# Optimization experiments

Measured on AMD Instinct MI355X. Metric: run time of the kernel, lower is better.

Reference implementation:

```python
import jax, jax.numpy as jnp
import numpy as np

N_SRC = 50000
N_DST = 50000
E = 640000
D_IN = 128
D_OUT = 128
H = 4
D_HEAD = D_OUT // H


def setup_inputs() -> dict:
    key = jax.random.key(0)
    k1, k2, k3, k4, k5, k6 = jax.random.split(key, 6)
    src_feat = jax.random.normal(k1, (N_SRC, D_IN), dtype=jnp.float32)
    dst_feat = jax.random.normal(k2, (N_DST, D_IN), dtype=jnp.float32)
    src_idx = jax.random.randint(k3, (E,), 0, N_SRC)
    dst_idx = jax.random.randint(k4, (E,), 0, N_DST)
    edge_index = jnp.stack([src_idx, dst_idx], axis=0)  # [2, E]
    # nn.Linear(d_in, d_out, bias=False): store as [d_in, d_out] so h = x @ W
    W = jax.random.normal(k5, (D_IN, D_OUT), dtype=jnp.float32) * (1.0 / np.sqrt(D_IN))
    # nn.Linear(2*d_head, 1, bias=False): attention vector of length 2*d_head
    a = jax.random.normal(k6, (2 * D_HEAD,), dtype=jnp.float32) * (1.0 / np.sqrt(2 * D_HEAD))
    return {"src_feat": src_feat, "dst_feat": dst_feat, "edge_index": edge_index,
            "W": W, "a": a, "num_dst": N_DST}


def reference(src_feat, dst_feat, edge_index, W, a, num_dst):
    # Dropout in eval mode (identity).
    d_out = W.shape[1]
    d_head = d_out // H
    src_idx = edge_index[0]
    dst_idx = edge_index[1]

    h_src = (src_feat @ W).reshape(-1, H, d_head)  # [N_src, H, d_head]
    h_dst = (dst_feat @ W).reshape(-1, H, d_head)  # [N_dst, H, d_head]
    h_src_e = h_src[src_idx]                        # [E, H, d_head]
    h_dst_e = h_dst[dst_idx]                        # [E, H, d_head]

    # a^T [h_src || h_dst] == h_src . a_src + h_dst . a_dst (shared across heads)
    a_src, a_dst = a[:d_head], a[d_head:]
    e = jax.nn.elu(jnp.einsum('ehd,d->eh', h_src_e, a_src)
                   + jnp.einsum('ehd,d->eh', h_dst_e, a_dst))  # [E, H]

    # Segment softmax over edges grouped by destination node.
    e_max = jax.ops.segment_max(e, dst_idx, num_segments=num_dst)      # [N_dst, H]
    exp_e = jnp.exp(e - e_max[dst_idx])
    denom = jax.ops.segment_sum(exp_e, dst_idx, num_segments=num_dst)  # [N_dst, H]
    alpha = exp_e / (denom[dst_idx] + 1e-12)                           # [E, H]

    # Scatter-add of weighted messages.
    out = jax.ops.segment_sum(alpha[..., None] * h_src_e, dst_idx,
                              num_segments=num_dst)                    # [N_dst, H, d_head]
    return out.reshape(num_dst, d_out)
```

## Files before the change

kernel.cpp:

```cpp
#include <hip/hip_runtime.h>
#include <math.h>

constexpr int N_SRC_ = 50000;
constexpr int N_DST_ = 50000;
constexpr int N_TOT_ = 100000;
constexpr int E_     = 640000;
constexpr int D_     = 128;
constexpr int CAP_   = 64;
constexpr int NTILE  = (N_SRC_ + 31) / 32;
constexpr int MMB    = (NTILE + 3) / 4;
constexpr int NCHUNK = (E_ + 2047) / 2048;
constexpr int SCB    = NCHUNK * 8;
constexpr int DPR    = N_DST_ / 8;

typedef float f32x4  __attribute__((ext_vector_type(4)));
typedef short bf16x8 __attribute__((ext_vector_type(8)));

union U4 { unsigned int u[4]; bf16x8 v; };

static __device__ __forceinline__ unsigned short f2bf_rne(float f) {
    unsigned int x = __float_as_uint(f);
    return (unsigned short)((x + 0x7FFFu + ((x >> 16) & 1u)) >> 16);
}

__global__ __launch_bounds__(256) void k_prep(
    const float* __restrict__ W, const float* __restrict__ a,
    unsigned short* __restrict__ wt, float* __restrict__ va)
{
    int tid = blockIdx.x * 256 + threadIdx.x;
    if (tid >= 136 * 16) return;
    int n = tid >> 4, c = tid & 15;
    if (n < 128) {
        int slot = c ^ (n & 15);
        size_t base = (size_t)n * 128 + slot * 8;
#pragma unroll
        for (int j = 0; j < 8; ++j) {
            int k = c * 8 + j;
            wt[base + j] = f2bf_rne(W[(size_t)k * 128 + n]);
        }
    } else {
        int col = n - 128, half = col >> 2, hd = col & 3;
#pragma unroll
        for (int j = 0; j < 8; ++j) {
            int k = c * 8 + j;
            float acc = 0.f;
            for (int c2 = 0; c2 < 32; ++c2)
                acc += W[(size_t)k * 128 + hd * 32 + c2] * a[half * 32 + c2];
            va[(size_t)k * 8 + col] = acc;
        }
    }
}

__global__ __launch_bounds__(256) void k_s2(
    const float* __restrict__ src, const float* __restrict__ dst,
    const float* __restrict__ va, float* __restrict__ s)
{
    const int gw = (blockIdx.x * 256 + threadIdx.x) >> 6;
    const int lane = threadIdx.x & 63;
    const int l32 = lane & 31, hf = lane >> 5;

    float4 vs[4], vd[4];
#pragma unroll
    for (int j = 0; j < 4; ++j) {
        const float* vp = va + (size_t)(4 * l32 + j) * 8;
        vs[j] = *(const float4*)vp;
        vd[j] = *(const float4*)(vp + 4);
    }

    for (int p = gw; p < N_TOT_ / 2; p += 2048) {
        int node = p * 2 + hf;
        bool is_src = node < N_SRC_;
        const float* f = is_src ? src + (size_t)node * D_
                                : dst + (size_t)(node - N_SRC_) * D_;
        float4 x = *(const float4*)(f + l32 * 4);
        float4 v0 = is_src ? vs[0] : vd[0];
        float4 v1 = is_src ? vs[1] : vd[1];
        float4 v2 = is_src ? vs[2] : vd[2];
        float4 v3 = is_src ? vs[3] : vd[3];
        float a0 = x.x * v0.x + x.y * v1.x + x.z * v2.x + x.w * v3.x;
        float a1 = x.x * v0.y + x.y * v1.y + x.z * v2.y + x.w * v3.y;
        float a2 = x.x * v0.z + x.y * v1.z + x.z * v2.z + x.w * v3.z;
        float a3 = x.x * v0.w + x.y * v1.w + x.z * v2.w + x.w * v3.w;
#pragma unroll
        for (int m = 1; m < 32; m <<= 1) {
            a0 += __shfl_xor(a0, m, 64);
            a1 += __shfl_xor(a1, m, 64);
            a2 += __shfl_xor(a2, m, 64);
            a3 += __shfl_xor(a3, m, 64);
        }
        if (l32 == 0)
            *(float4*)&s[(size_t)node * 4] = make_float4(a0, a1, a2, a3);
    }
}

__global__ __launch_bounds__(256) void k_mms(
    const float* __restrict__ src, const unsigned short* __restrict__ wt,
    const int* __restrict__ src_idx, const int* __restrict__ dst_idx,
    const float* __restrict__ s,
    int* __restrict__ cursor, uint4* __restrict__ bucket,
    unsigned int* __restrict__ h)
{
    if (blockIdx.x >= MMB) {
        int bid = (int)blockIdx.x - MMB;
        int r = bid & 7;
        int ebase = (bid >> 3) * 2048 + threadIdx.x;
#pragma unroll
        for (int ii = 0; ii < 8; ++ii) {
            int e = ebase + ii * 256;
            if (e >= E_) break;
            int dn = dst_idx[e];
            if (dn / DPR != r) continue;
            int sn = src_idx[e];
            float4 vsv = *(const float4*)&s[(size_t)sn * 4];
            float4 vdv = *(const float4*)&s[(size_t)(N_SRC_ + dn) * 4];
            float x0 = vsv.x + vdv.x, x1 = vsv.y + vdv.y;
            float x2 = vsv.z + vdv.z, x3 = vsv.w + vdv.w;
            float w0 = __expf(x0 > 0.f ? x0 : (__expf(x0) - 1.f));
            float w1 = __expf(x1 > 0.f ? x1 : (__expf(x1) - 1.f));
            float w2 = __expf(x2 > 0.f ? x2 : (__expf(x2) - 1.f));
            float w3 = __expf(x3 > 0.f ? x3 : (__expf(x3) - 1.f));
            uint4 ent;
            ent.x = (unsigned int)sn;
            ent.y = (unsigned int)f2bf_rne(w0) | ((unsigned int)f2bf_rne(w1) << 16);
            ent.z = (unsigned int)f2bf_rne(w2) | ((unsigned int)f2bf_rne(w3) << 16);
            ent.w = 0u;
            int pos = atomicAdd(&cursor[dn], 1);
            if (pos < CAP_) bucket[(size_t)dn * CAP_ + pos] = ent;
        }
        return;
    }

    __shared__ unsigned short wl[128 * 128];
    const int t = threadIdx.x;
    {
        const float4* gw = (const float4*)wt;
        float4* sw = (float4*)wl;
#pragma unroll
        for (int i = 0; i < 8; ++i) sw[t + 256 * i] = gw[t + 256 * i];
    }
    __syncthreads();

    const int wid = t >> 6, lane = t & 63;
    const int g = lane >> 4, sidx = lane & 15;
    const int wtile = blockIdx.x * 4 + wid;
    if (wtile >= NTILE) return;
    const int base = wtile * 32;
    const int r0 = base + sidx;
    const int r1g = base + 16 + sidx;
    const int r1 = (r1g < N_SRC_) ? r1g : 0;
    const float* p0 = src + (size_t)r0 * D_;
    const float* p1 = src + (size_t)r1 * D_;

    f32x4 acc[2][8];
#pragma unroll
    for (int m = 0; m < 2; ++m)
#pragma unroll
        for (int nf = 0; nf < 8; ++nf) acc[m][nf] = (f32x4)0.f;

#pragma unroll
    for (int ks = 0; ks < 4; ++ks) {
        const int k0 = ks * 32 + g * 8;
        bf16x8 af[2];
#pragma unroll
        for (int m = 0; m < 2; ++m) {
            const float* p = m ? p1 : p0;
            float4 v0 = *(const float4*)(p + k0);
            float4 v1 = *(const float4*)(p + k0 + 4);
            float f[8] = {v0.x, v0.y, v0.z, v0.w, v1.x, v1.y, v1.z, v1.w};
            U4 P;
#pragma unroll
            for (int q = 0; q < 4; ++q)
                P.u[q] = (unsigned int)f2bf_rne(f[2 * q])
                       | ((unsigned int)f2bf_rne(f[2 * q + 1]) << 16);
            af[m] = P.v;
        }
#pragma unroll
        for (int nf = 0; nf < 8; ++nf) {
            const int n = nf * 16 + sidx;
            const int off = n * 128 + ((ks * 4 + g) ^ sidx) * 8;
            bf16x8 b = *(const bf16x8*)&wl[off];
            acc[0][nf] = __builtin_amdgcn_mfma_f32_16x16x32_bf16(af[0], b, acc[0][nf], 0, 0, 0);
            acc[1][nf] = __builtin_amdgcn_mfma_f32_16x16x32_bf16(af[1], b, acc[1][nf], 0, 0, 0);
        }
    }

#pragma unroll
    for (int m = 0; m < 2; ++m) {
        const int rowb = base + m * 16 + g * 4;
#pragma unroll
        for (int r = 0; r < 4; ++r) {
            const int row = rowb + r;
            if (row < N_SRC_) {
#pragma unroll
                for (int q = 0; q < 4; ++q) {
                    unsigned int val = (unsigned int)f2bf_rne(acc[m][2 * q][r])
                                     | ((unsigned int)f2bf_rne(acc[m][2 * q + 1][r]) << 16);
                    h[(size_t)row * 64 + q * 16 + sidx] = val;
                }
            }
        }
    }
}

__global__ __launch_bounds__(256) void k_gather(
    const unsigned int* __restrict__ h2, const int* __restrict__ cursor,
    const uint4* __restrict__ bucket, float* __restrict__ out)
{
    int wid = (blockIdx.x * 256 + threadIdx.x) >> 6;
    int lane = threadIdx.x & 63;
    if (wid >= N_DST_) return;
    int cnt = min(cursor[wid], CAP_);
    const int hd = lane >> 4;
    const int sub = lane & 15;
    const uint4* B = bucket + (size_t)wid * CAP_;

    auto wext = [&](const uint4& e) {
        unsigned int u = (hd & 2) ? e.z : e.y;
        return __uint_as_float((hd & 1) ? (u & 0xFFFF0000u) : (u << 16));
    };

    float2 A0 = make_float2(0.f, 0.f), A1 = A0, A2 = A0, A3 = A0;
    float d0 = 0.f, d1 = 0.f, d2 = 0.f, d3 = 0.f;
    int i = 0;
    for (; i + 4 <= cnt; i += 4) {
        uint4 e0 = B[i], e1 = B[i + 1], e2 = B[i + 2], e3 = B[i + 3];
        unsigned int v0 = h2[(size_t)e0.x * 64 + lane];
        unsigned int v1 = h2[(size_t)e1.x * 64 + lane];
        unsigned int v2 = h2[(size_t)e2.x * 64 + lane];
        unsigned int v3 = h2[(size_t)e3.x * 64 + lane];
        float w0 = wext(e0), w1 = wext(e1), w2 = wext(e2), w3 = wext(e3);
        d0 += w0; d1 += w1; d2 += w2; d3 += w3;
        A0.x = fmaf(w0, __uint_as_float(v0 << 16), A0.x);
        A0.y = fmaf(w0, __uint_as_float(v0 & 0xFFFF0000u), A0.y);
        A1.x = fmaf(w1, __uint_as_float(v1 << 16), A1.x);
        A1.y = fmaf(w1, __uint_as_float(v1 & 0xFFFF0000u), A1.y);
        A2.x = fmaf(w2, __uint_as_float(v2 << 16), A2.x);
        A2.y = fmaf(w2, __uint_as_float(v2 & 0xFFFF0000u), A2.y);
        A3.x = fmaf(w3, __uint_as_float(v3 << 16), A3.x);
        A3.y = fmaf(w3, __uint_as_float(v3 & 0xFFFF0000u), A3.y);
    }
    for (; i < cnt; ++i) {
        uint4 e = B[i];
        unsigned int v = h2[(size_t)e.x * 64 + lane];
        float w = wext(e);
        d0 += w;
        A0.x = fmaf(w, __uint_as_float(v << 16), A0.x);
        A0.y = fmaf(w, __uint_as_float(v & 0xFFFF0000u), A0.y);
    }

    float den = (d0 + d1) + (d2 + d3);
    float2 acc = make_float2((A0.x + A1.x) + (A2.x + A3.x),
                             (A0.y + A1.y) + (A2.y + A3.y));
    float inv = 1.f / (den + 1e-12f);
    out[(size_t)wid * D_ + 32 * hd + sub]      = acc.x * inv;
    out[(size_t)wid * D_ + 32 * hd + sub + 16] = acc.y * inv;
}

extern "C" void kernel_launch(void* const* d_in, const int* in_sizes, int n_in,
                              void* d_out, int out_size, void* d_ws, size_t ws_size,
                              hipStream_t stream)
{
    const float* src_feat = (const float*)d_in[0];
    const float* dst_feat = (const float*)d_in[1];
    const int*   edge     = (const int*)d_in[2];
    const int*   src_idx  = edge;
    const int*   dst_idx  = edge + E_;
    const float* W        = (const float*)d_in[3];
    const float* a        = (const float*)d_in[4];
    float*       out      = (float*)d_out;

    char* p = (char*)d_ws;
    auto alloc = [&](size_t bytes) {
        char* r = p;
        p += (bytes + 255) & ~(size_t)255;
        return r;
    };
    unsigned int* h    = (unsigned int*)alloc((size_t)N_SRC_ * 64 * 4);
    float*  s          = (float*)alloc((size_t)N_TOT_ * 4 * sizeof(float));
    int*    cursor     = (int*)alloc((size_t)N_DST_ * sizeof(int));
    uint4*  bucket     = (uint4*)alloc((size_t)N_DST_ * CAP_ * sizeof(uint4));
    unsigned short* wt = (unsigned short*)alloc((size_t)128 * 128 * 2);
    float*  va         = (float*)alloc((size_t)128 * 8 * sizeof(float));

    hipMemsetAsync(cursor, 0, (size_t)N_DST_ * sizeof(int), stream);

    k_prep<<<(136 * 16 + 255) / 256, 256, 0, stream>>>(W, a, wt, va);
    k_s2<<<512, 256, 0, stream>>>(src_feat, dst_feat, va, s);
    k_mms<<<MMB + SCB, 256, 0, stream>>>(src_feat, wt, src_idx, dst_idx, s,
                                         cursor, bucket, h);
    k_gather<<<(N_DST_ * 64 + 255) / 256, 256, 0, stream>>>(
        h, cursor, bucket, out);
}
```

Measured before the change: 216.7 us.

## Fold prep into projection kernels, split scatter out, deepen gather unroll

Removes the separate weight-prep kernel and the cursor memset. Each s2v block now recomputes W·a in shared memory and zeroes the cursors, and each matmul block converts W to swizzled bf16 in LDS directly. The edge scatter moves from a co-scheduled part of the matmul launch, which filtered edges by destination range over 8 passes, to its own one-edge-per-thread kernel, which cuts the redundant index reads. The gather loop is unrolled to 8 outstanding row loads. The cost is redundant per-block W·a and W-transpose work with strided global reads, and the scatter no longer overlaps the matmul.

```diff
diff --git a/kernel.cpp b/kernel.cpp
--- a/kernel.cpp
+++ b/kernel.cpp
@@ -9,9 +9,6 @@
 constexpr int CAP_   = 64;
 constexpr int NTILE  = (N_SRC_ + 31) / 32;
 constexpr int MMB    = (NTILE + 3) / 4;
-constexpr int NCHUNK = (E_ + 2047) / 2048;
-constexpr int SCB    = NCHUNK * 8;
-constexpr int DPR    = N_DST_ / 8;
 
 typedef float f32x4  __attribute__((ext_vector_type(4)));
 typedef short bf16x8 __attribute__((ext_vector_type(8)));
@@ -23,48 +20,38 @@
     return (unsigned short)((x + 0x7FFFu + ((x >> 16) & 1u)) >> 16);
 }
 
-__global__ __launch_bounds__(256) void k_prep(
+__global__ __launch_bounds__(256) void k_s2v(
+    const float* __restrict__ src, const float* __restrict__ dst,
     const float* __restrict__ W, const float* __restrict__ a,
-    unsigned short* __restrict__ wt, float* __restrict__ va)
-{
-    int tid = blockIdx.x * 256 + threadIdx.x;
-    if (tid >= 136 * 16) return;
-    int n = tid >> 4, c = tid & 15;
-    if (n < 128) {
-        int slot = c ^ (n & 15);
-        size_t base = (size_t)n * 128 + slot * 8;
-#pragma unroll
-        for (int j = 0; j < 8; ++j) {
-            int k = c * 8 + j;
-            wt[base + j] = f2bf_rne(W[(size_t)k * 128 + n]);
-        }
-    } else {
-        int col = n - 128, half = col >> 2, hd = col & 3;
-#pragma unroll
-        for (int j = 0; j < 8; ++j) {
-            int k = c * 8 + j;
-            float acc = 0.f;
-            for (int c2 = 0; c2 < 32; ++c2)
-                acc += W[(size_t)k * 128 + hd * 32 + c2] * a[half * 32 + c2];
-            va[(size_t)k * 8 + col] = acc;
-        }
-    }
-}
-
-__global__ __launch_bounds__(256) void k_s2(
-    const float* __restrict__ src, const float* __restrict__ dst,
-    const float* __restrict__ va, float* __restrict__ s)
-{
-    const int gw = (blockIdx.x * 256 + threadIdx.x) >> 6;
-    const int lane = threadIdx.x & 63;
+    float* __restrict__ s, int* __restrict__ cursor)
+{
+    __shared__ float val[128 * 8];
+    const int t = threadIdx.x;
+
+    int cid = blockIdx.x * 256 + t;
+    if (cid < N_DST_) cursor[cid] = 0;
+
+#pragma unroll
+    for (int j = 0; j < 4; ++j) {
+        int pair = t * 4 + j;
+        int k = pair >> 3, col = pair & 7;
+        int half = col >> 2, hd = col & 3;
+        float acc = 0.f;
+        for (int c2 = 0; c2 < 32; ++c2)
+            acc += W[(size_t)k * 128 + hd * 32 + c2] * a[half * 32 + c2];
+        val[k * 8 + col] = acc;
+    }
+    __syncthreads();
+
+    const int gw = (blockIdx.x * 256 + t) >> 6;
+    const int lane = t & 63;
     const int l32 = lane & 31, hf = lane >> 5;
 
     float4 vs[4], vd[4];
 #pragma unroll
     for (int j = 0; j < 4; ++j) {
-        const float* vp = va + (size_t)(4 * l32 + j) * 8;
-        vs[j] = *(const float4*)vp;
-        vd[j] = *(const float4*)(vp + 4);
+        vs[j] = *(const float4*)&val[(4 * l32 + j) * 8];
+        vd[j] = *(const float4*)&val[(4 * l32 + j) * 8 + 4];
     }
 
     for (int p = gw; p < N_TOT_ / 2; p += 2048) {
@@ -93,50 +80,28 @@
     }
 }
 
-__global__ __launch_bounds__(256) void k_mms(
-    const float* __restrict__ src, const unsigned short* __restrict__ wt,
-    const int* __restrict__ src_idx, const int* __restrict__ dst_idx,
-    const float* __restrict__ s,
-    int* __restrict__ cursor, uint4* __restrict__ bucket,
+__global__ __launch_bounds__(256) void k_mm(
+    const float* __restrict__ src, const float* __restrict__ W,
     unsigned int* __restrict__ h)
 {
-    if (blockIdx.x >= MMB) {
-        int bid = (int)blockIdx.x - MMB;
-        int r = bid & 7;
-        int ebase = (bid >> 3) * 2048 + threadIdx.x;
-#pragma unroll
-        for (int ii = 0; ii < 8; ++ii) {
-            int e = ebase + ii * 256;
-            if (e >= E_) break;
-            int dn = dst_idx[e];
-            if (dn / DPR != r) continue;
-            int sn = src_idx[e];
-            float4 vsv = *(const float4*)&s[(size_t)sn * 4];
-            float4 vdv = *(const float4*)&s[(size_t)(N_SRC_ + dn) * 4];
-            float x0 = vsv.x + vdv.x, x1 = vsv.y + vdv.y;
-            float x2 = vsv.z + vdv.z, x3 = vsv.w + vdv.w;
-            float w0 = __expf(x0 > 0.f ? x0 : (__expf(x0) - 1.f));
-            float w1 = __expf(x1 > 0.f ? x1 : (__expf(x1) - 1.f));
-            float w2 = __expf(x2 > 0.f ? x2 : (__expf(x2) - 1.f));
-            float w3 = __expf(x3 > 0.f ? x3 : (__expf(x3) - 1.f));
-            uint4 ent;
-            ent.x = (unsigned int)sn;
-            ent.y = (unsigned int)f2bf_rne(w0) | ((unsigned int)f2bf_rne(w1) << 16);
-            ent.z = (unsigned int)f2bf_rne(w2) | ((unsigned int)f2bf_rne(w3) << 16);
-            ent.w = 0u;
-            int pos = atomicAdd(&cursor[dn], 1);
-            if (pos < CAP_) bucket[(size_t)dn * CAP_ + pos] = ent;
-        }
-        return;
-    }
-
     __shared__ unsigned short wl[128 * 128];
     const int t = threadIdx.x;
     {
-        const float4* gw = (const float4*)wt;
-        float4* sw = (float4*)wl;
-#pragma unroll
-        for (int i = 0; i < 8; ++i) sw[t + 256 * i] = gw[t + 256 * i];
+        const int n = t >> 1, half = t & 1;
+#pragma unroll
+        for (int c8 = 0; c8 < 8; ++c8) {
+            int c = half * 8 + c8;
+            U4 P;
+#pragma unroll
+            for (int q = 0; q < 4; ++q) {
+                float f0 = W[(size_t)(c * 8 + 2 * q) * 128 + n];
+                float f1 = W[(size_t)(c * 8 + 2 * q + 1) * 128 + n];
+                P.u[q] = (unsigned int)f2bf_rne(f0)
+                       | ((unsigned int)f2bf_rne(f1) << 16);
+            }
+            int slot = c ^ (n & 15);
+            *(bf16x8*)&wl[n * 128 + slot * 8] = P.v;
+        }
     }
     __syncthreads();
 
@@ -202,6 +167,30 @@
     }
 }
 
+__global__ __launch_bounds__(256) void k_scatter(
+    const int* __restrict__ src_idx, const int* __restrict__ dst_idx,
+    const float* __restrict__ s,
+    int* __restrict__ cursor, uint4* __restrict__ bucket)
+{
+    int e = blockIdx.x * 256 + threadIdx.x;
+    int sn = src_idx[e], dn = dst_idx[e];
+    float4 vsv = *(const float4*)&s[(size_t)sn * 4];
+    float4 vdv = *(const float4*)&s[(size_t)(N_SRC_ + dn) * 4];
+    float x0 = vsv.x + vdv.x, x1 = vsv.y + vdv.y;
+    float x2 = vsv.z + vdv.z, x3 = vsv.w + vdv.w;
+    float w0 = __expf(x0 > 0.f ? x0 : (__expf(x0) - 1.f));
+    float w1 = __expf(x1 > 0.f ? x1 : (__expf(x1) - 1.f));
+    float w2 = __expf(x2 > 0.f ? x2 : (__expf(x2) - 1.f));
+    float w3 = __expf(x3 > 0.f ? x3 : (__expf(x3) - 1.f));
+    uint4 ent;
+    ent.x = (unsigned int)sn;
+    ent.y = (unsigned int)f2bf_rne(w0) | ((unsigned int)f2bf_rne(w1) << 16);
+    ent.z = (unsigned int)f2bf_rne(w2) | ((unsigned int)f2bf_rne(w3) << 16);
+    ent.w = 0u;
+    int pos = atomicAdd(&cursor[dn], 1);
+    if (pos < CAP_) bucket[(size_t)dn * CAP_ + pos] = ent;
+}
+
 __global__ __launch_bounds__(256) void k_gather(
     const unsigned int* __restrict__ h2, const int* __restrict__ cursor,
     const uint4* __restrict__ bucket, float* __restrict__ out)
@@ -219,38 +208,53 @@
         return __uint_as_float((hd & 1) ? (u & 0xFFFF0000u) : (u << 16));
     };
 
-    float2 A0 = make_float2(0.f, 0.f), A1 = A0, A2 = A0, A3 = A0;
-    float d0 = 0.f, d1 = 0.f, d2 = 0.f, d3 = 0.f;
+    float2 A[4] = {make_float2(0.f, 0.f), make_float2(0.f, 0.f),
+                   make_float2(0.f, 0.f), make_float2(0.f, 0.f)};
+    float dacc[4] = {0.f, 0.f, 0.f, 0.f};
+
     int i = 0;
+    for (; i + 8 <= cnt; i += 8) {
+        uint4 e[8];
+        unsigned int v[8];
+#pragma unroll
+        for (int j = 0; j < 8; ++j) e[j] = B[i + j];
+#pragma unroll
+        for (int j = 0; j < 8; ++j) v[j] = h2[(size_t)e[j].x * 64 + lane];
+#pragma unroll
+        for (int j = 0; j < 8; ++j) {
+            float w = wext(e[j]);
+            dacc[j & 3] += w;
+            A[j & 3].x = fmaf(w, __uint_as_float(v[j] << 16), A[j & 3].x);
+            A[j & 3].y = fmaf(w, __uint_as_float(v[j] & 0xFFFF0000u), A[j & 3].y);
+        }
+    }
     for (; i + 4 <= cnt; i += 4) {
-        uint4 e0 = B[i], e1 = B[i + 1], e2 = B[i + 2], e3 = B[i + 3];
-        unsigned int v0 = h2[(size_t)e0.x * 64 + lane];
-        unsigned int v1 = h2[(size_t)e1.x * 64 + lane];
-        unsigned int v2 = h2[(size_t)e2.x * 64 + lane];
-        unsigned int v3 = h2[(size_t)e3.x * 64 + lane];
-        float w0 = wext(e0), w1 = wext(e1), w2 = wext(e2), w3 = wext(e3);
-        d0 += w0; d1 += w1; d2 += w2; d3 += w3;
-        A0.x = fmaf(w0, __uint_as_float(v0 << 16), A0.x);
-        A0.y = fmaf(w0, __uint_as_float(v0 & 0xFFFF0000u), A0.y);
-        A1.x = fmaf(w1, __uint_as_float(v1 << 16), A1.x);
-        A1.y = fmaf(w1, __uint_as_float(v1 & 0xFFFF0000u), A1.y);
-        A2.x = fmaf(w2, __uint_as_float(v2 << 16), A2.x);
-        A2.y = fmaf(w2, __uint_as_float(v2 & 0xFFFF0000u), A2.y);
-        A3.x = fmaf(w3, __uint_as_float(v3 << 16), A3.x);
-        A3.y = fmaf(w3, __uint_as_float(v3 & 0xFFFF0000u), A3.y);
+        uint4 e[4];
+        unsigned int v[4];
+#pragma unroll
+        for (int j = 0; j < 4; ++j) e[j] = B[i + j];
+#pragma unroll
+        for (int j = 0; j < 4; ++j) v[j] = h2[(size_t)e[j].x * 64 + lane];
+#pragma unroll
+        for (int j = 0; j < 4; ++j) {
+            float w = wext(e[j]);
+            dacc[j] += w;
+            A[j].x = fmaf(w, __uint_as_float(v[j] << 16), A[j].x);
+            A[j].y = fmaf(w, __uint_as_float(v[j] & 0xFFFF0000u), A[j].y);
+        }
     }
     for (; i < cnt; ++i) {
         uint4 e = B[i];
         unsigned int v = h2[(size_t)e.x * 64 + lane];
         float w = wext(e);
-        d0 += w;
-        A0.x = fmaf(w, __uint_as_float(v << 16), A0.x);
-        A0.y = fmaf(w, __uint_as_float(v & 0xFFFF0000u), A0.y);
-    }
-
-    float den = (d0 + d1) + (d2 + d3);
-    float2 acc = make_float2((A0.x + A1.x) + (A2.x + A3.x),
-                             (A0.y + A1.y) + (A2.y + A3.y));
+        dacc[0] += w;
+        A[0].x = fmaf(w, __uint_as_float(v << 16), A[0].x);
+        A[0].y = fmaf(w, __uint_as_float(v & 0xFFFF0000u), A[0].y);
+    }
+
+    float den = (dacc[0] + dacc[1]) + (dacc[2] + dacc[3]);
+    float2 acc = make_float2((A[0].x + A[1].x) + (A[2].x + A[3].x),
+                             (A[0].y + A[1].y) + (A[2].y + A[3].y));
     float inv = 1.f / (den + 1e-12f);
     out[(size_t)wid * D_ + 32 * hd + sub]      = acc.x * inv;
     out[(size_t)wid * D_ + 32 * hd + sub + 16] = acc.y * inv;
@@ -275,19 +279,14 @@
         p += (bytes + 255) & ~(size_t)255;
         return r;
     };
-    unsigned int* h    = (unsigned int*)alloc((size_t)N_SRC_ * 64 * 4);
-    float*  s          = (float*)alloc((size_t)N_TOT_ * 4 * sizeof(float));
-    int*    cursor     = (int*)alloc((size_t)N_DST_ * sizeof(int));
-    uint4*  bucket     = (uint4*)alloc((size_t)N_DST_ * CAP_ * sizeof(uint4));
-    unsigned short* wt = (unsigned short*)alloc((size_t)128 * 128 * 2);
-    float*  va         = (float*)alloc((size_t)128 * 8 * sizeof(float));
-
-    hipMemsetAsync(cursor, 0, (size_t)N_DST_ * sizeof(int), stream);
-
-    k_prep<<<(136 * 16 + 255) / 256, 256, 0, stream>>>(W, a, wt, va);
-    k_s2<<<512, 256, 0, stream>>>(src_feat, dst_feat, va, s);
-    k_mms<<<MMB + SCB, 256, 0, stream>>>(src_feat, wt, src_idx, dst_idx, s,
-                                         cursor, bucket, h);
+    unsigned int* h = (unsigned int*)alloc((size_t)N_SRC_ * 64 * 4);
+    float* s        = (float*)alloc((size_t)N_TOT_ * 4 * sizeof(float));
+    int*   cursor   = (int*)alloc((size_t)N_DST_ * sizeof(int));
+    uint4* bucket   = (uint4*)alloc((size_t)N_DST_ * CAP_ * sizeof(uint4));
+
+    k_s2v<<<512, 256, 0, stream>>>(src_feat, dst_feat, W, a, s, cursor);
+    k_mm<<<MMB, 256, 0, stream>>>(src_feat, W, h);
+    k_scatter<<<E_ / 256, 256, 0, stream>>>(src_idx, dst_idx, s, cursor, bucket);
     k_gather<<<(N_DST_ * 64 + 255) / 256, 256, 0, stream>>>(
         h, cursor, bucket, out);
 }
```

New measurement: 215.3 us. No clear change (-0.6%).
